# Kernel optimization log

Hardware: AMD Instinct MI355X
Metric: run time of the kernel (lower is better)

The kernel has to match this reference:

```python
import math
import jax, jax.numpy as jnp
import numpy as np

EMBED_DIM = 1024
NUM_HEADS = 16
HEAD_DIM = EMBED_DIM // NUM_HEADS  # 64


def setup_inputs() -> dict:
    key = jax.random.key(0)
    kx, kq, ko = jax.random.split(key, 3)
    B, S, D = 4, 1024, EMBED_DIM
    x = jax.random.normal(kx, (B, S, D), dtype=jnp.float32)
    # xavier_uniform for Dense kernels, zeros for biases
    def xavier(k, shape):
        fan_in, fan_out = shape[0], shape[1]
        limit = math.sqrt(6.0 / (fan_in + fan_out))
        return jax.random.uniform(k, shape, jnp.float32, -limit, limit)
    W_qkv = xavier(kq, (D, 3 * D))
    b_qkv = jnp.zeros((3 * D,), jnp.float32)
    W_o = xavier(ko, (D, D))
    b_o = jnp.zeros((D,), jnp.float32)
    return {"x": x, "W_qkv": W_qkv, "b_qkv": b_qkv, "W_o": W_o, "b_o": b_o}


def reference(x, W_qkv, b_qkv, W_o, b_o):
    B, S, D = x.shape
    H, hd = NUM_HEADS, HEAD_DIM
    qkv = x @ W_qkv + b_qkv                         # [B,S,3D]
    qkv = qkv.reshape(B, S, H, 3 * hd).transpose(0, 2, 1, 3)  # [B,H,S,3hd]
    q, k, v = jnp.split(qkv, 3, axis=-1)            # each [B,H,S,hd]
    attn_logits = jnp.einsum('bhqd,bhkd->bhqk', q, k) / math.sqrt(hd)
    attention = jax.nn.softmax(attn_logits, axis=-1)  # [B,H,S,S]
    values = jnp.einsum('bhqk,bhkd->bhqd', attention, v)
    values = values.transpose(0, 2, 1, 3).reshape(B, S, D)
    o = values @ W_o + b_o
    return (o, attention)
```

## Files before the change

kernel.cpp:

```cpp
#include <hip/hip_runtime.h>

#define B_   4
#define S_   1024
#define D_   1024
#define H_   16
#define HD_  64

typedef __bf16 bf16_t;
typedef __attribute__((ext_vector_type(8))) __bf16 bf16x8;
typedef __attribute__((ext_vector_type(4))) float f32x4;

#define MFMA16(a, b, c) __builtin_amdgcn_mfma_f32_16x16x32_bf16((a), (b), (c), 0, 0, 0)

__device__ inline unsigned short f2bf(float f) {
    unsigned int u = __builtin_bit_cast(unsigned int, f);
    u += 0x7FFFu + ((u >> 16) & 1u);
    return (unsigned short)(u >> 16);
}

__device__ inline bf16x8 ld_frag(const unsigned short* p) {
    uint4 u = *(const uint4*)p;
    return __builtin_bit_cast(bf16x8, u);
}

__device__ inline void gload_lds16(const unsigned short* g, unsigned short* l) {
    __builtin_amdgcn_global_load_lds(
        (const __attribute__((address_space(1))) void*)g,
        (__attribute__((address_space(3))) void*)l,
        16, 0, 0);
}

__global__ __launch_bounds__(256) void convert_f32_bf16(
    const float* __restrict__ in, unsigned short* __restrict__ out)
{
    const size_t idx = (size_t)blockIdx.x * 256 + threadIdx.x;
    float4 v = *(const float4*)(in + idx * 4);
    unsigned short* o = out + idx * 4;
    ushort4 r;
    r.x = f2bf(v.x); r.y = f2bf(v.y); r.z = f2bf(v.z); r.w = f2bf(v.w);
    *(ushort4*)o = r;
}

__global__ __launch_bounds__(256) void transpose_f32_bf16(
    const float* __restrict__ in, unsigned short* __restrict__ out,
    int K, int N)
{
    __shared__ float T[64][65];
    const int tid = threadIdx.x;
    const int k0 = blockIdx.y * 64, n0 = blockIdx.x * 64;
#pragma unroll
    for (int i = 0; i < 4; ++i) {
        int c = tid + i * 256;
        int row = c >> 4, col = (c & 15) << 2;
        float4 v = *(const float4*)(in + (size_t)(k0 + row) * N + n0 + col);
        T[row][col + 0] = v.x; T[row][col + 1] = v.y;
        T[row][col + 2] = v.z; T[row][col + 3] = v.w;
    }
    __syncthreads();
#pragma unroll
    for (int i = 0; i < 4; ++i) {
        int c = tid + i * 256;
        int nr = c >> 4, kc = (c & 15) << 2;
        ushort4 r;
        r.x = f2bf(T[kc + 0][nr]); r.y = f2bf(T[kc + 1][nr]);
        r.z = f2bf(T[kc + 2][nr]); r.w = f2bf(T[kc + 3][nr]);
        *(ushort4*)(out + (size_t)(n0 + nr) * K + k0 + kc) = r;
    }
}

__global__ __launch_bounds__(256) void transpose_v_bf16(
    const unsigned short* __restrict__ v,
    unsigned short* __restrict__ vt)
{
    __shared__ unsigned short T[64][65];
    const int tid = threadIdx.x;
    const int kt = blockIdx.x, bh = blockIdx.y;
    const int b = bh >> 4, h = bh & 15;
#pragma unroll
    for (int i = 0; i < 2; ++i) {
        const int c = tid + i * 256;
        const int key = c >> 3, off = (c & 7) << 3;
        uint4 u = *(const uint4*)(v + (size_t)(b * 1024 + kt * 64 + key) * 1024 + h * 64 + off);
        union { uint4 u4; unsigned short us[8]; } uu; uu.u4 = u;
#pragma unroll
        for (int t = 0; t < 8; ++t) T[key][off + t] = uu.us[t];
    }
    __syncthreads();
#pragma unroll
    for (int i = 0; i < 16; ++i) {
        const int c = tid + i * 256;
        const int dim = c >> 6, key = c & 63;
        vt[((size_t)bh * 64 + dim) * 1024 + kt * 64 + key] = T[key][dim];
    }
}

template<int MODE>
__global__ __launch_bounds__(256) void gemm_bf16(
    const unsigned short* __restrict__ A,
    const unsigned short* __restrict__ Bt,
    const float* __restrict__ bias,
    unsigned short* __restrict__ qk,
    unsigned short* __restrict__ vnat,
    float* __restrict__ out,
    int K, int N)
{
    __shared__ unsigned short Alds[128][64];
    __shared__ unsigned short Blds[128][64];
    const int tid  = threadIdx.x;
    const int l    = tid & 63, w = tid >> 6;
    const int wm   = w >> 1, wn = w & 1;
    const int quad = l >> 4, n16 = l & 15;
    const int bm = blockIdx.y * 128, bn = blockIdx.x * 128;

    const int lrow = l >> 3;
    const int lcol = (l & 7) << 3;

    const f32x4 zero4 = {0.f, 0.f, 0.f, 0.f};
    f32x4 acc[4][4];
#pragma unroll
    for (int i = 0; i < 4; ++i)
#pragma unroll
        for (int j = 0; j < 4; ++j) acc[i][j] = zero4;

    for (int k0 = 0; k0 < K; k0 += 64) {
#pragma unroll
        for (int i = 0; i < 4; ++i) {
            const int c8  = (w * 4 + i) * 8;
            const int row = c8 + lrow;
            gload_lds16(A  + (size_t)(bm + row) * K + k0 + lcol, &Alds[c8][0]);
            gload_lds16(Bt + (size_t)(bn + row) * K + k0 + lcol, &Blds[c8][0]);
        }
        __syncthreads();
#pragma unroll
        for (int kk = 0; kk < 2; ++kk) {
            const int kc = kk * 32 + quad * 8;
            bf16x8 af[4], bfv[4];
#pragma unroll
            for (int i = 0; i < 4; ++i) af[i]  = ld_frag(&Alds[wm * 64 + i * 16 + n16][kc]);
#pragma unroll
            for (int j = 0; j < 4; ++j) bfv[j] = ld_frag(&Blds[wn * 64 + j * 16 + n16][kc]);
#pragma unroll
            for (int i = 0; i < 4; ++i)
#pragma unroll
                for (int j = 0; j < 4; ++j)
                    acc[i][j] = MFMA16(af[i], bfv[j], acc[i][j]);
        }
        __syncthreads();
    }

#pragma unroll
    for (int j = 0; j < 4; ++j) {
        const int col0 = bn + wn * 64 + j * 16;
        const int col  = col0 + n16;
        const float bv = bias ? bias[col] : 0.f;
        if (MODE == 0) {
            const int head = col0 / 192;
            const int rem  = col0 % 192;
            if (rem < 128) {
                const float sc = (rem < 64) ? 0.125f : 1.0f;
#pragma unroll
                for (int i = 0; i < 4; ++i)
#pragma unroll
                    for (int r = 0; r < 4; ++r) {
                        int row = bm + wm * 64 + i * 16 + quad * 4 + r;
                        qk[(size_t)row * 2048 + head * 128 + rem + n16] =
                            f2bf((acc[i][j][r] + bv) * sc);
                    }
            } else {
                const int dcol = head * 64 + (rem - 128) + n16;
#pragma unroll
                for (int i = 0; i < 4; ++i)
#pragma unroll
                    for (int r = 0; r < 4; ++r) {
                        int row = bm + wm * 64 + i * 16 + quad * 4 + r;
                        vnat[(size_t)row * 1024 + dcol] = f2bf(acc[i][j][r] + bv);
                    }
            }
        } else {
#pragma unroll
            for (int i = 0; i < 4; ++i)
#pragma unroll
                for (int r = 0; r < 4; ++r) {
                    int row = bm + wm * 64 + i * 16 + quad * 4 + r;
                    out[(size_t)row * N + col] = acc[i][j][r] + bv;
                }
        }
    }
}

__global__ __launch_bounds__(256) void attn_fused(
    const unsigned short* __restrict__ qk,
    const unsigned short* __restrict__ vt,
    float* __restrict__ attn,
    unsigned short* __restrict__ values)
{
    __shared__ unsigned short Plds[16][1032];
    __shared__ float redbuf[2][4][16];

    const int qb = blockIdx.x, bh = blockIdx.y;
    const int b = bh >> 4, h = bh & 15;
    const int tid = threadIdx.x, l = tid & 63, w = tid >> 6;
    const int quad = l >> 4, n16 = l & 15;

    bf16x8 qf[2];
    {
        const unsigned short* qbase =
            qk + (size_t)(b * 1024 + qb * 16 + n16) * 2048 + h * 128 + quad * 8;
        qf[0] = ld_frag(qbase);
        qf[1] = ld_frag(qbase + 32);
    }

    const f32x4 zero4 = {0.f, 0.f, 0.f, 0.f};
    f32x4 c[16];
#pragma unroll
    for (int s = 0; s < 16; ++s) c[s] = zero4;

    const unsigned short* kbase = qk + (size_t)(b * 1024) * 2048 + h * 128 + 64;
#pragma unroll
    for (int s = 0; s < 16; ++s) {
        const unsigned short* kr = kbase + (size_t)(s * 64 + w * 16 + n16) * 2048;
        bf16x8 k0f = ld_frag(kr + quad * 8);
        bf16x8 k1f = ld_frag(kr + 32 + quad * 8);
        c[s] = MFMA16(qf[0], k0f, c[s]);
        c[s] = MFMA16(qf[1], k1f, c[s]);
    }

    float mx[4] = {-1e30f, -1e30f, -1e30f, -1e30f};
#pragma unroll
    for (int s = 0; s < 16; ++s)
#pragma unroll
        for (int r = 0; r < 4; ++r)
            mx[r] = fmaxf(mx[r], c[s][r]);
#pragma unroll
    for (int off = 1; off <= 8; off <<= 1)
#pragma unroll
        for (int r = 0; r < 4; ++r)
            mx[r] = fmaxf(mx[r], __shfl_xor(mx[r], off, 64));
    if (n16 == 0)
#pragma unroll
        for (int r = 0; r < 4; ++r) redbuf[0][w][quad * 4 + r] = mx[r];
    __syncthreads();
#pragma unroll
    for (int r = 0; r < 4; ++r) {
        const int row = quad * 4 + r;
        float m = redbuf[0][0][row];
        m = fmaxf(m, redbuf[0][1][row]);
        m = fmaxf(m, redbuf[0][2][row]);
        m = fmaxf(m, redbuf[0][3][row]);
        mx[r] = m;
    }

    float sm[4] = {0.f, 0.f, 0.f, 0.f};
#pragma unroll
    for (int s = 0; s < 16; ++s)
#pragma unroll
        for (int r = 0; r < 4; ++r) {
            float e = __expf(c[s][r] - mx[r]);
            c[s][r] = e;
            sm[r] += e;
        }
#pragma unroll
    for (int off = 1; off <= 8; off <<= 1)
#pragma unroll
        for (int r = 0; r < 4; ++r)
            sm[r] += __shfl_xor(sm[r], off, 64);
    if (n16 == 0)
#pragma unroll
        for (int r = 0; r < 4; ++r) redbuf[1][w][quad * 4 + r] = sm[r];
    __syncthreads();
    float inv[4];
#pragma unroll
    for (int r = 0; r < 4; ++r) {
        const int row = quad * 4 + r;
        inv[r] = 1.f / (redbuf[1][0][row] + redbuf[1][1][row] +
                        redbuf[1][2][row] + redbuf[1][3][row]);
    }

    float* abase = attn + ((size_t)bh * 1024 + qb * 16) * 1024;
#pragma unroll
    for (int s = 0; s < 16; ++s)
#pragma unroll
        for (int r = 0; r < 4; ++r) {
            const float a = c[s][r] * inv[r];
            const int row = quad * 4 + r;
            const int key = s * 64 + w * 16 + n16;
            abase[(size_t)row * 1024 + key] = a;
            Plds[row][key] = f2bf(a);
        }
    __syncthreads();

    f32x4 o = zero4;
    const unsigned short* vbase = vt + (size_t)bh * 65536 +
                                  (size_t)(w * 16 + n16) * 1024;
#pragma unroll
    for (int s = 0; s < 16; ++s) {
#pragma unroll
        for (int kk = 0; kk < 2; ++kk) {
            bf16x8 pf = ld_frag(&Plds[n16][s * 64 + kk * 32 + quad * 8]);
            bf16x8 vf = ld_frag(vbase + s * 64 + kk * 32 + quad * 8);
            o = MFMA16(pf, vf, o);
        }
    }

#pragma unroll
    for (int r = 0; r < 4; ++r) {
        const int row = quad * 4 + r;
        values[(size_t)(b * 1024 + qb * 16 + row) * 1024 + h * 64 + w * 16 + n16] =
            f2bf(o[r]);
    }
}

extern "C" void kernel_launch(void* const* d_in, const int* in_sizes, int n_in,
                              void* d_out, int out_size, void* d_ws, size_t ws_size,
                              hipStream_t stream)
{
    const float* x     = (const float*)d_in[0];
    const float* W_qkv = (const float*)d_in[1];
    const float* b_qkv = (const float*)d_in[2];
    const float* W_o   = (const float*)d_in[3];
    const float* b_o   = (const float*)d_in[4];

    float* o_out    = (float*)d_out;
    float* attn_out = o_out + (size_t)B_ * S_ * D_;

    const size_t M1 = 1ull << 20;
    unsigned short* ws      = (unsigned short*)d_ws;
    unsigned short* x_bf    = ws;
    unsigned short* wqkvt   = ws + 4 * M1;
    unsigned short* wot     = ws + 7 * M1;
    unsigned short* qkbuf   = ws + 8 * M1;
    unsigned short* vtbuf   = ws + 16 * M1;
    unsigned short* valbuf  = ws + 20 * M1;

    convert_f32_bf16<<<4096, 256, 0, stream>>>(x, x_bf);
    transpose_f32_bf16<<<dim3(3072 / 64, 1024 / 64), 256, 0, stream>>>(W_qkv, wqkvt, 1024, 3072);
    transpose_f32_bf16<<<dim3(1024 / 64, 1024 / 64), 256, 0, stream>>>(W_o, wot, 1024, 1024);

    gemm_bf16<0><<<dim3(3072 / 128, 4096 / 128), 256, 0, stream>>>(
        x_bf, wqkvt, b_qkv, qkbuf, valbuf, nullptr, 1024, 3072);

    transpose_v_bf16<<<dim3(S_ / 64, B_ * H_), 256, 0, stream>>>(valbuf, vtbuf);

    attn_fused<<<dim3(S_ / 16, B_ * H_), 256, 0, stream>>>(
        qkbuf, vtbuf, attn_out, valbuf);

    gemm_bf16<1><<<dim3(1024 / 128, 4096 / 128), 256, 0, stream>>>(
        valbuf, wot, b_o, nullptr, nullptr, o_out, 1024, 1024);
}
```

Measured before the change: 497.0 us.

## Stage K/V tiles through per-wave double-buffered LDS and pad GEMM LDS tiles

In the attention kernel, K and V fragments are no longer loaded straight from global memory with strided per-lane reads. Each wave now loads row-coalesced 16x64 tiles into its own double-buffered LDS region, prefetching the next tile while it computes the current one. The GEMM drops the direct global-to-LDS loads in favour of plain register-staged uint4 copies into LDS tiles padded to 72 columns, which avoids bank conflicts on fragment reads. This adds LDS traffic and register pressure, and the per-wave buffers have no explicit wave barrier; the code relies on lockstep execution within a wave.

```diff
diff --git a/kernel.cpp b/kernel.cpp
--- a/kernel.cpp
+++ b/kernel.cpp
@@ -21,13 +21,6 @@
 __device__ inline bf16x8 ld_frag(const unsigned short* p) {
     uint4 u = *(const uint4*)p;
     return __builtin_bit_cast(bf16x8, u);
-}
-
-__device__ inline void gload_lds16(const unsigned short* g, unsigned short* l) {
-    __builtin_amdgcn_global_load_lds(
-        (const __attribute__((address_space(1))) void*)g,
-        (__attribute__((address_space(3))) void*)l,
-        16, 0, 0);
 }
 
 __global__ __launch_bounds__(256) void convert_f32_bf16(
@@ -104,17 +97,14 @@
     float* __restrict__ out,
     int K, int N)
 {
-    __shared__ unsigned short Alds[128][64];
-    __shared__ unsigned short Blds[128][64];
+    __shared__ unsigned short Alds[128][72];
+    __shared__ unsigned short Blds[128][72];
     const int tid  = threadIdx.x;
     const int l    = tid & 63, w = tid >> 6;
     const int wm   = w >> 1, wn = w & 1;
     const int quad = l >> 4, n16 = l & 15;
     const int bm = blockIdx.y * 128, bn = blockIdx.x * 128;
 
-    const int lrow = l >> 3;
-    const int lcol = (l & 7) << 3;
-
     const f32x4 zero4 = {0.f, 0.f, 0.f, 0.f};
     f32x4 acc[4][4];
 #pragma unroll
@@ -125,10 +115,10 @@
     for (int k0 = 0; k0 < K; k0 += 64) {
 #pragma unroll
         for (int i = 0; i < 4; ++i) {
-            const int c8  = (w * 4 + i) * 8;
-            const int row = c8 + lrow;
-            gload_lds16(A  + (size_t)(bm + row) * K + k0 + lcol, &Alds[c8][0]);
-            gload_lds16(Bt + (size_t)(bn + row) * K + k0 + lcol, &Blds[c8][0]);
+            int c = tid + i * 256;
+            int row = c >> 3, off = (c & 7) << 3;
+            *(uint4*)&Alds[row][off] = *(const uint4*)(A + (size_t)(bm + row) * K + k0 + off);
+            *(uint4*)&Blds[row][off] = *(const uint4*)(Bt + (size_t)(bn + row) * K + k0 + off);
         }
         __syncthreads();
 #pragma unroll
@@ -194,6 +184,7 @@
     float* __restrict__ attn,
     unsigned short* __restrict__ values)
 {
+    __shared__ unsigned short KVw[4][2][16][72];
     __shared__ unsigned short Plds[16][1032];
     __shared__ float redbuf[2][4][16];
 
@@ -201,6 +192,9 @@
     const int b = bh >> 4, h = bh & 15;
     const int tid = threadIdx.x, l = tid & 63, w = tid >> 6;
     const int quad = l >> 4, n16 = l & 15;
+
+    const int prow = l >> 3;
+    const int poff = (l & 7) << 3;
 
     bf16x8 qf[2];
     {
@@ -215,14 +209,30 @@
 #pragma unroll
     for (int s = 0; s < 16; ++s) c[s] = zero4;
 
-    const unsigned short* kbase = qk + (size_t)(b * 1024) * 2048 + h * 128 + 64;
-#pragma unroll
+    const unsigned short* kwbase =
+        qk + (size_t)(b * 1024 + w * 16) * 2048 + h * 128 + 64;
+    {
+        uint4 r0 = *(const uint4*)(kwbase + (size_t)prow * 2048 + poff);
+        uint4 r1 = *(const uint4*)(kwbase + (size_t)(prow + 8) * 2048 + poff);
+        *(uint4*)&KVw[w][0][prow][poff]     = r0;
+        *(uint4*)&KVw[w][0][prow + 8][poff] = r1;
+    }
     for (int s = 0; s < 16; ++s) {
-        const unsigned short* kr = kbase + (size_t)(s * 64 + w * 16 + n16) * 2048;
-        bf16x8 k0f = ld_frag(kr + quad * 8);
-        bf16x8 k1f = ld_frag(kr + 32 + quad * 8);
+        uint4 n0, n1;
+        if (s < 15) {
+            const unsigned short* p = kwbase + (size_t)(s + 1) * 64 * 2048;
+            n0 = *(const uint4*)(p + (size_t)prow * 2048 + poff);
+            n1 = *(const uint4*)(p + (size_t)(prow + 8) * 2048 + poff);
+        }
+        const int pb = s & 1;
+        bf16x8 k0f = ld_frag(&KVw[w][pb][n16][quad * 8]);
+        bf16x8 k1f = ld_frag(&KVw[w][pb][n16][32 + quad * 8]);
         c[s] = MFMA16(qf[0], k0f, c[s]);
         c[s] = MFMA16(qf[1], k1f, c[s]);
+        if (s < 15) {
+            *(uint4*)&KVw[w][pb ^ 1][prow][poff]     = n0;
+            *(uint4*)&KVw[w][pb ^ 1][prow + 8][poff] = n1;
+        }
     }
 
     float mx[4] = {-1e30f, -1e30f, -1e30f, -1e30f};
@@ -290,15 +300,31 @@
     __syncthreads();
 
     f32x4 o = zero4;
-    const unsigned short* vbase = vt + (size_t)bh * 65536 +
-                                  (size_t)(w * 16 + n16) * 1024;
-#pragma unroll
+    const unsigned short* vwbase = vt + (size_t)bh * 65536 +
+                                   (size_t)(w * 16) * 1024;
+    {
+        uint4 r0 = *(const uint4*)(vwbase + (size_t)prow * 1024 + poff);
+        uint4 r1 = *(const uint4*)(vwbase + (size_t)(prow + 8) * 1024 + poff);
+        *(uint4*)&KVw[w][0][prow][poff]     = r0;
+        *(uint4*)&KVw[w][0][prow + 8][poff] = r1;
+    }
     for (int s = 0; s < 16; ++s) {
+        uint4 n0, n1;
+        if (s < 15) {
+            const unsigned short* p = vwbase + (s + 1) * 64;
+            n0 = *(const uint4*)(p + (size_t)prow * 1024 + poff);
+            n1 = *(const uint4*)(p + (size_t)(prow + 8) * 1024 + poff);
+        }
+        const int pb = s & 1;
 #pragma unroll
         for (int kk = 0; kk < 2; ++kk) {
             bf16x8 pf = ld_frag(&Plds[n16][s * 64 + kk * 32 + quad * 8]);
-            bf16x8 vf = ld_frag(vbase + s * 64 + kk * 32 + quad * 8);
+            bf16x8 vf = ld_frag(&KVw[w][pb][n16][kk * 32 + quad * 8]);
             o = MFMA16(pf, vf, o);
+        }
+        if (s < 15) {
+            *(uint4*)&KVw[w][pb ^ 1][prow][poff]     = n0;
+            *(uint4*)&KVw[w][pb ^ 1][prow + 8][poff] = n1;
         }
     }
 
```

Measured after the change: 442.2 us. 11.0% less time.
